# Optimization experiments

Hardware: AMD Instinct MI355X
Metric: run time of the kernel (lower is better)

Reference implementation:

```python
import jax, jax.numpy as jnp
import numpy as np

B, T, D, H = 8, 256, 12, 4
NQ = 12                      # n_qubits_ffn == ffn_dim
NL_ATTN, NL_FFN = 2, 2
EPS = 1e-5
C64 = jnp.complex64


def _z_signs(n):
    # [n, 2**n] sign table: wire 0 is the most-significant bit of the flat index
    idx = np.arange(2 ** n)
    bits = (idx[None, :] >> (n - 1 - np.arange(n)[:, None])) & 1
    return jnp.asarray(1 - 2 * bits, dtype=jnp.float32)


def _apply_1q(state, gate, n, w):
    # state [N, 2**n]; gate [2,2] (shared) or [N,2,2] (per-token)
    a, b = 2 ** w, 2 ** (n - w - 1)
    s = state.reshape(-1, a, 2, b)
    if gate.ndim == 2:
        s = jnp.einsum('ij,najb->naib', gate, s)
    else:
        s = jnp.einsum('nij,najb->naib', gate, s)
    return s.reshape(-1, 2 ** n)


def _apply_cnot(state, n, c, t):
    s = state.reshape((-1,) + (2,) * n)
    ac, at = 1 + c, 1 + t
    s0 = jnp.take(s, 0, axis=ac)
    s1 = jnp.take(s, 1, axis=ac)
    s1 = jnp.flip(s1, axis=at - 1 if at > ac else at)  # flip target where control==1
    s = jnp.stack([s0, s1], axis=ac)
    return s.reshape(-1, 2 ** n)


def _rx_batched(theta):  # theta [N] -> [N,2,2]
    c = jnp.cos(theta / 2).astype(C64)
    s = jnp.sin(theta / 2).astype(C64)
    return jnp.stack([c, -1j * s, -1j * s, c], axis=-1).reshape(-1, 2, 2)


def _rx_scalar(theta):
    c = jnp.cos(theta / 2).astype(C64)
    s = jnp.sin(theta / 2).astype(C64)
    return jnp.stack([c, -1j * s, -1j * s, c]).reshape(2, 2)


def _ry_scalar(theta):
    c = jnp.cos(theta / 2)
    s = jnp.sin(theta / 2)
    return jnp.stack([c, -s, s, c]).reshape(2, 2).astype(C64)


def _qcircuit(angles, thetas, n, n_layers, param_gate):
    # angles [N, n] encoder RX rotations; thetas [n] trainable gate params
    N = angles.shape[0]
    state = jnp.zeros((N, 2 ** n), C64).at[:, 0].set(1.0)
    for w in range(n):                       # GeneralEncoder: RX(x_w) on wire w
        state = _apply_1q(state, _rx_batched(angles[:, w]), n, w)
    for w in range(n):                       # trainable RX/RY per wire
        state = _apply_1q(state, param_gate(thetas[w]), n, w)
    for _ in range(n_layers - 1):            # CNOT entangling ring
        for w in range(n - 1):
            state = _apply_cnot(state, n, w, w + 1)
        state = _apply_cnot(state, n, n - 1, 0)
    probs = jnp.abs(state) ** 2
    return probs @ _z_signs(n).T             # MeasureAll(PauliZ) -> [N, n]


def _layer_norm(x, g, b):
    m = x.mean(-1, keepdims=True)
    v = ((x - m) ** 2).mean(-1, keepdims=True)
    return (x - m) * jax.lax.rsqrt(v + EPS) * g + b


def _mha(x, mask, Wi, bi, Wo, bo):
    qkv = x @ Wi.T + bi
    q, k, v = jnp.split(qkv, 3, axis=-1)
    hd = D // H
    sh = lambda t: t.reshape(B, T, H, hd).transpose(0, 2, 1, 3)
    q, k, v = sh(q), sh(k), sh(v)
    scores = jnp.einsum('bhqd,bhkd->bhqk', q, k) / float(np.sqrt(hd))
    scores = jnp.where(mask[:, None, None, :] != 0, -jnp.inf, scores)
    attn = jax.nn.softmax(scores, axis=-1)
    out = jnp.einsum('bhqk,bhkd->bhqd', attn, v).transpose(0, 2, 1, 3).reshape(B, T, D)
    return out @ Wo.T + bo


def setup_inputs() -> dict:
    key = jax.random.key(0)
    ks = jax.random.split(key, 12)
    g = lambda i, shape, sc: (jax.random.normal(ks[i], shape, jnp.float32) * sc)
    return {
        'x': jax.random.normal(ks[0], (B, T, D), jnp.float32),
        'in_proj_w': g(1, (3 * D, D), 0.3),
        'in_proj_b': g(2, (3 * D,), 0.02),
        'out_proj_w': g(3, (D, D), 0.3),
        'out_proj_b': g(4, (D,), 0.02),
        'attn_theta': jax.random.uniform(ks[5], (D,), jnp.float32, -np.pi, np.pi),
        'lin1_w': g(6, (NQ, D), 0.3),
        'lin1_b': g(7, (NQ,), 0.02),
        'ffn_theta': jax.random.uniform(ks[8], (NQ,), jnp.float32, -np.pi, np.pi),
        'lin2_w': g(9, (D, NQ), 0.3),
        'lin2_b': g(10, (D,), 0.02),
        'ln1_g': jnp.ones((D,), jnp.float32),
        'ln1_b': jnp.zeros((D,), jnp.float32),
        'ln2_g': jnp.ones((D,), jnp.float32),
        'ln2_b': jnp.zeros((D,), jnp.float32),
        'mask': jnp.zeros((B, T), jnp.int32),
    }


def reference(x, in_proj_w, in_proj_b, out_proj_w, out_proj_b, attn_theta,
              lin1_w, lin1_b, ffn_theta, lin2_w, lin2_b,
              ln1_g, ln1_b, ln2_g, ln2_b, mask):
    # quantum multi-head attention (dropout/noise are identity in eval)
    attn_cls = _mha(x, mask, in_proj_w, in_proj_b, out_proj_w, out_proj_b)
    attn_q = _qcircuit(attn_cls.reshape(B * T, D), attn_theta, D, NL_ATTN,
                       _rx_scalar).reshape(B, T, D)
    x1 = _layer_norm(x + attn_q, ln1_g, ln1_b)
    # quantum feed-forward
    q_in = x1 @ lin1_w.T + lin1_b                       # [B,T,NQ]
    ffn_q = _qcircuit(q_in.reshape(B * T, NQ), ffn_theta, NQ, NL_FFN,
                      _ry_scalar).reshape(B, T, NQ)
    ffn_out = jax.nn.relu(ffn_q @ lin2_w.T + lin2_b)    # [B,T,D]
    return _layer_norm(x1 + ffn_out, ln2_g, ln2_b)
```

## Files before the change

kernel.cpp:

```cpp
#include <hip/hip_runtime.h>
#include <math.h>

#define BB 8
#define TT 256
#define DD 12
#define HH 4
#define HDIM 3

__global__ __launch_bounds__(TT) void attn_kernel(
    const float* __restrict__ x,
    const float* __restrict__ wi,
    const float* __restrict__ bi,
    const int*   __restrict__ mask,
    float* __restrict__ headout)
{
    const int b = blockIdx.x / HH;
    const int h = blockIdx.x % HH;
    const int t = threadIdx.x;

    __shared__ float kk[HDIM][TT];
    __shared__ float vv[HDIM][TT];
    __shared__ float mbias[TT];

    float xv[DD];
    const float* xr = x + (b * TT + t) * DD;
#pragma unroll
    for (int j = 0; j < DD; ++j) xv[j] = xr[j];

    float q[HDIM];
#pragma unroll
    for (int d = 0; d < HDIM; ++d) {
        const int rq = h * HDIM + d;
        const int rk = DD + h * HDIM + d;
        const int rv = 2 * DD + h * HDIM + d;
        float aq = bi[rq], ak = bi[rk], av = bi[rv];
#pragma unroll
        for (int j = 0; j < DD; ++j) {
            aq = fmaf(wi[rq * DD + j], xv[j], aq);
            ak = fmaf(wi[rk * DD + j], xv[j], ak);
            av = fmaf(wi[rv * DD + j], xv[j], av);
        }
        q[d] = aq;
        kk[d][t] = ak;
        vv[d][t] = av;
    }
    mbias[t] = (mask[b * TT + t] != 0) ? -INFINITY : 0.0f;
    __syncthreads();

    const float scale = 0.57735026918962576f;

    float m = -INFINITY;
#pragma unroll 4
    for (int k = 0; k < TT; ++k) {
        float s = fmaf(q[0], kk[0][k], fmaf(q[1], kk[1][k], q[2] * kk[2][k])) * scale + mbias[k];
        m = fmaxf(m, s);
    }
    float sum = 0.f, o0 = 0.f, o1 = 0.f, o2 = 0.f;
#pragma unroll 4
    for (int k = 0; k < TT; ++k) {
        float s = fmaf(q[0], kk[0][k], fmaf(q[1], kk[1][k], q[2] * kk[2][k])) * scale + mbias[k];
        float e = __expf(s - m);
        sum += e;
        o0 = fmaf(e, vv[0][k], o0);
        o1 = fmaf(e, vv[1][k], o1);
        o2 = fmaf(e, vv[2][k], o2);
    }
    const float inv = 1.0f / sum;
    float* orow = headout + (b * TT + t) * DD + h * HDIM;
    orow[0] = o0 * inv;
    orow[1] = o1 * inv;
    orow[2] = o2 * inv;
}

__device__ __forceinline__ void ring_measure(const float* z, float* outp)
{
    float pref = 1.0f;
#pragma unroll
    for (int j = 0; j < DD; ++j) { pref *= z[j]; outp[j] = pref; }
    float suf = 1.0f;
#pragma unroll
    for (int j = 1; j < DD; ++j) suf *= z[j];
    outp[0] = suf;
}

__device__ __forceinline__ void layer_norm(float* v, const float* __restrict__ g,
                                           const float* __restrict__ b)
{
    float mean = 0.f;
#pragma unroll
    for (int j = 0; j < DD; ++j) mean += v[j];
    mean *= (1.0f / DD);
    float var = 0.f;
#pragma unroll
    for (int j = 0; j < DD; ++j) { float d = v[j] - mean; var = fmaf(d, d, var); }
    var *= (1.0f / DD);
    const float r = rsqrtf(var + 1e-5f);
#pragma unroll
    for (int j = 0; j < DD; ++j) v[j] = (v[j] - mean) * r * g[j] + b[j];
}

__global__ __launch_bounds__(64) void fused_tail_kernel(
    const float* __restrict__ x,
    const float* __restrict__ headout,
    const float* __restrict__ wo, const float* __restrict__ bo,
    const float* __restrict__ th_a,
    const float* __restrict__ w1, const float* __restrict__ b1,
    const float* __restrict__ th_f,
    const float* __restrict__ w2, const float* __restrict__ b2,
    const float* __restrict__ g1, const float* __restrict__ be1,
    const float* __restrict__ g2, const float* __restrict__ be2,
    float* __restrict__ out)
{
    const int n = blockIdx.x * blockDim.x + threadIdx.x;
    if (n >= BB * TT) return;

    float hv[DD];
    const float* ho = headout + n * DD;
#pragma unroll
    for (int j = 0; j < DD; ++j) hv[j] = ho[j];

    float ac[DD];
#pragma unroll
    for (int d = 0; d < DD; ++d) {
        float a = bo[d];
#pragma unroll
        for (int j = 0; j < DD; ++j) a = fmaf(wo[d * DD + j], hv[j], a);
        ac[d] = a;
    }

    float z[DD], aq[DD];
#pragma unroll
    for (int j = 0; j < DD; ++j) z[j] = cosf(ac[j] + th_a[j]);
    ring_measure(z, aq);

    float x1[DD];
    const float* xr = x + n * DD;
#pragma unroll
    for (int j = 0; j < DD; ++j) x1[j] = xr[j] + aq[j];
    layer_norm(x1, g1, be1);

    float qi[DD];
#pragma unroll
    for (int d = 0; d < DD; ++d) {
        float a = b1[d];
#pragma unroll
        for (int j = 0; j < DD; ++j) a = fmaf(w1[d * DD + j], x1[j], a);
        qi[d] = a;
    }

    float fq[DD];
#pragma unroll
    for (int j = 0; j < DD; ++j) z[j] = cosf(th_f[j]) * cosf(qi[j]);
    ring_measure(z, fq);

    float y[DD];
#pragma unroll
    for (int d = 0; d < DD; ++d) {
        float a = b2[d];
#pragma unroll
        for (int j = 0; j < DD; ++j) a = fmaf(w2[d * DD + j], fq[j], a);
        y[d] = fmaxf(a, 0.0f) + x1[d];
    }
    layer_norm(y, g2, be2);

    float* orow = out + n * DD;
#pragma unroll
    for (int j = 0; j < DD; ++j) orow[j] = y[j];
}

extern "C" void kernel_launch(void* const* d_in, const int* in_sizes, int n_in,
                              void* d_out, int out_size, void* d_ws, size_t ws_size,
                              hipStream_t stream)
{
    const float* x    = (const float*)d_in[0];
    const float* wi   = (const float*)d_in[1];
    const float* bi   = (const float*)d_in[2];
    const float* wo   = (const float*)d_in[3];
    const float* bo   = (const float*)d_in[4];
    const float* tha  = (const float*)d_in[5];
    const float* w1   = (const float*)d_in[6];
    const float* b1   = (const float*)d_in[7];
    const float* thf  = (const float*)d_in[8];
    const float* w2   = (const float*)d_in[9];
    const float* b2   = (const float*)d_in[10];
    const float* g1   = (const float*)d_in[11];
    const float* be1  = (const float*)d_in[12];
    const float* g2   = (const float*)d_in[13];
    const float* be2  = (const float*)d_in[14];
    const int*   mask = (const int*)d_in[15];
    float* out = (float*)d_out;
    float* headout = (float*)d_ws;

    attn_kernel<<<BB * HH, TT, 0, stream>>>(x, wi, bi, mask, headout);
    fused_tail_kernel<<<(BB * TT + 63) / 64, 64, 0, stream>>>(
        x, headout, wo, bo, tha, w1, b1, thf, w2, b2, g1, be1, g2, be2, out);
}
```

Measured before the change: 117.2 us.

## Use single-pass online softmax with packed float4 K/V and fast cosines

The attention loop becomes a one-pass online softmax with two independent accumulator chains, so the two passes over K are gone. K, V and the mask bias are packed into float4 shared-memory entries so each key needs one vector load. Scaling is folded into q. The tail kernel switches to float4 global loads and stores and replaces cosf with __cosf. The online softmax costs two exps per key instead of one, __cosf gives up some accuracy, and -INFINITY is swapped for a large finite negative value.

```diff
diff --git a/kernel.cpp b/kernel.cpp
--- a/kernel.cpp
+++ b/kernel.cpp
@@ -6,6 +6,7 @@
 #define DD 12
 #define HH 4
 #define HDIM 3
+#define MASK_NEG -3.0e38f
 
 __global__ __launch_bounds__(TT) void attn_kernel(
     const float* __restrict__ x,
@@ -18,16 +19,15 @@
     const int h = blockIdx.x % HH;
     const int t = threadIdx.x;
 
-    __shared__ float kk[HDIM][TT];
-    __shared__ float vv[HDIM][TT];
-    __shared__ float mbias[TT];
-
-    float xv[DD];
-    const float* xr = x + (b * TT + t) * DD;
-#pragma unroll
-    for (int j = 0; j < DD; ++j) xv[j] = xr[j];
-
-    float q[HDIM];
+    __shared__ float4 kk4[TT];
+    __shared__ float4 vv4[TT];
+
+    const float4* xr4 = (const float4*)(x + (b * TT + t) * DD);
+    const float4 p0 = xr4[0], p1 = xr4[1], p2 = xr4[2];
+    const float xv[DD] = {p0.x, p0.y, p0.z, p0.w, p1.x, p1.y, p1.z, p1.w,
+                          p2.x, p2.y, p2.z, p2.w};
+
+    float q[HDIM], kx[HDIM], vx[HDIM];
 #pragma unroll
     for (int d = 0; d < HDIM; ++d) {
         const int rq = h * HDIM + d;
@@ -40,36 +40,53 @@
             ak = fmaf(wi[rk * DD + j], xv[j], ak);
             av = fmaf(wi[rv * DD + j], xv[j], av);
         }
-        q[d] = aq;
-        kk[d][t] = ak;
-        vv[d][t] = av;
-    }
-    mbias[t] = (mask[b * TT + t] != 0) ? -INFINITY : 0.0f;
+        q[d] = aq; kx[d] = ak; vx[d] = av;
+    }
+    const float mb = (mask[b * TT + t] != 0) ? MASK_NEG : 0.0f;
+    kk4[t] = make_float4(kx[0], kx[1], kx[2], mb);
+    vv4[t] = make_float4(vx[0], vx[1], vx[2], 0.0f);
     __syncthreads();
 
     const float scale = 0.57735026918962576f;
-
-    float m = -INFINITY;
+    const float qs0 = q[0] * scale, qs1 = q[1] * scale, qs2 = q[2] * scale;
+
+    float mA = MASK_NEG, sumA = 0.f, aA0 = 0.f, aA1 = 0.f, aA2 = 0.f;
+    float mB = MASK_NEG, sumB = 0.f, aB0 = 0.f, aB1 = 0.f, aB2 = 0.f;
 #pragma unroll 4
-    for (int k = 0; k < TT; ++k) {
-        float s = fmaf(q[0], kk[0][k], fmaf(q[1], kk[1][k], q[2] * kk[2][k])) * scale + mbias[k];
-        m = fmaxf(m, s);
-    }
-    float sum = 0.f, o0 = 0.f, o1 = 0.f, o2 = 0.f;
-#pragma unroll 4
-    for (int k = 0; k < TT; ++k) {
-        float s = fmaf(q[0], kk[0][k], fmaf(q[1], kk[1][k], q[2] * kk[2][k])) * scale + mbias[k];
-        float e = __expf(s - m);
-        sum += e;
-        o0 = fmaf(e, vv[0][k], o0);
-        o1 = fmaf(e, vv[1][k], o1);
-        o2 = fmaf(e, vv[2][k], o2);
-    }
+    for (int k = 0; k < TT / 2; ++k) {
+        const float4 kA = kk4[k];
+        const float4 kB = kk4[k + TT / 2];
+        const float sA = fmaf(qs0, kA.x, fmaf(qs1, kA.y, qs2 * kA.z)) + kA.w;
+        const float sB = fmaf(qs0, kB.x, fmaf(qs1, kB.y, qs2 * kB.z)) + kB.w;
+        const float4 vA = vv4[k];
+        const float4 vB = vv4[k + TT / 2];
+
+        const float mAn = fmaxf(mA, sA);
+        const float cA  = __expf(mA - mAn);
+        const float eA  = __expf(sA - mAn);
+        sumA = fmaf(sumA, cA, eA);
+        aA0 = fmaf(aA0, cA, eA * vA.x);
+        aA1 = fmaf(aA1, cA, eA * vA.y);
+        aA2 = fmaf(aA2, cA, eA * vA.z);
+        mA = mAn;
+
+        const float mBn = fmaxf(mB, sB);
+        const float cB  = __expf(mB - mBn);
+        const float eB  = __expf(sB - mBn);
+        sumB = fmaf(sumB, cB, eB);
+        aB0 = fmaf(aB0, cB, eB * vB.x);
+        aB1 = fmaf(aB1, cB, eB * vB.y);
+        aB2 = fmaf(aB2, cB, eB * vB.z);
+        mB = mBn;
+    }
+    const float m  = fmaxf(mA, mB);
+    const float cA = __expf(mA - m), cB = __expf(mB - m);
+    const float sum = sumA * cA + sumB * cB;
     const float inv = 1.0f / sum;
     float* orow = headout + (b * TT + t) * DD + h * HDIM;
-    orow[0] = o0 * inv;
-    orow[1] = o1 * inv;
-    orow[2] = o2 * inv;
+    orow[0] = (aA0 * cA + aB0 * cB) * inv;
+    orow[1] = (aA1 * cA + aB1 * cB) * inv;
+    orow[2] = (aA2 * cA + aB2 * cB) * inv;
 }
 
 __device__ __forceinline__ void ring_measure(const float* z, float* outp)
@@ -114,10 +131,10 @@
     const int n = blockIdx.x * blockDim.x + threadIdx.x;
     if (n >= BB * TT) return;
 
-    float hv[DD];
-    const float* ho = headout + n * DD;
-#pragma unroll
-    for (int j = 0; j < DD; ++j) hv[j] = ho[j];
+    const float4* hr4 = (const float4*)(headout + n * DD);
+    const float4 h0 = hr4[0], h1 = hr4[1], h2 = hr4[2];
+    const float hv[DD] = {h0.x, h0.y, h0.z, h0.w, h1.x, h1.y, h1.z, h1.w,
+                          h2.x, h2.y, h2.z, h2.w};
 
     float ac[DD];
 #pragma unroll
@@ -130,13 +147,15 @@
 
     float z[DD], aq[DD];
 #pragma unroll
-    for (int j = 0; j < DD; ++j) z[j] = cosf(ac[j] + th_a[j]);
+    for (int j = 0; j < DD; ++j) z[j] = __cosf(ac[j] + th_a[j]);
     ring_measure(z, aq);
 
-    float x1[DD];
-    const float* xr = x + n * DD;
-#pragma unroll
-    for (int j = 0; j < DD; ++j) x1[j] = xr[j] + aq[j];
+    const float4* xr4 = (const float4*)(x + n * DD);
+    const float4 x0 = xr4[0], x1q = xr4[1], x2q = xr4[2];
+    float x1[DD] = {x0.x, x0.y, x0.z, x0.w, x1q.x, x1q.y, x1q.z, x1q.w,
+                    x2q.x, x2q.y, x2q.z, x2q.w};
+#pragma unroll
+    for (int j = 0; j < DD; ++j) x1[j] += aq[j];
     layer_norm(x1, g1, be1);
 
     float qi[DD];
@@ -150,7 +169,7 @@
 
     float fq[DD];
 #pragma unroll
-    for (int j = 0; j < DD; ++j) z[j] = cosf(th_f[j]) * cosf(qi[j]);
+    for (int j = 0; j < DD; ++j) z[j] = __cosf(th_f[j]) * __cosf(qi[j]);
     ring_measure(z, fq);
 
     float y[DD];
@@ -163,9 +182,10 @@
     }
     layer_norm(y, g2, be2);
 
-    float* orow = out + n * DD;
-#pragma unroll
-    for (int j = 0; j < DD; ++j) orow[j] = y[j];
+    float4* or4 = (float4*)(out + n * DD);
+    or4[0] = make_float4(y[0], y[1], y[2],  y[3]);
+    or4[1] = make_float4(y[4], y[5], y[6],  y[7]);
+    or4[2] = make_float4(y[8], y[9], y[10], y[11]);
 }
 
 extern "C" void kernel_launch(void* const* d_in, const int* in_sizes, int n_in,
```

Measured after the change: 103.5 us. -11.7%, faster.
